# Kernel optimization log

Hardware: AMD Instinct MI355X
Metric: run time of the kernel (lower is better)

Reference implementation:

```python
import jax, jax.numpy as jnp
import numpy as np

N = 20000


def _gcn_conv(x, edge_index, W, b):
    # add self loops
    n = x.shape[0]
    loops = jnp.arange(n, dtype=edge_index.dtype)
    row = jnp.concatenate([edge_index[0], loops])
    col = jnp.concatenate([edge_index[1], loops])
    # linear
    x = x @ W + b  # [N, C_out]
    # symmetric degree norm: deg computed over col (targets)
    deg = jax.ops.segment_sum(jnp.ones_like(col, dtype=x.dtype), col, num_segments=n)
    dinv = jnp.where(deg > 0, deg ** -0.5, 0.0)
    norm = dinv[row] * dinv[col]  # [E+N]
    # gather-scale-scatter (aggr='add' into col)
    msgs = norm[:, None] * x[row]  # [E+N, C_out]
    return jax.ops.segment_sum(msgs, col, num_segments=n)


def setup_inputs() -> dict:
    key = jax.random.key(0)
    k1, k2, k3, k4, k5, k6 = jax.random.split(key, 6)
    in_c, out_c = 256, 128
    hid = 2 * out_c
    x = jax.random.normal(k1, (N, in_c), dtype=jnp.float32)
    edge_index = jax.random.randint(k2, (2, 640000), 0, N, dtype=jnp.int64)
    s1 = 1.0 / np.sqrt(in_c)
    s2 = 1.0 / np.sqrt(hid)
    W1 = jax.random.uniform(k3, (in_c, hid), jnp.float32, -s1, s1)
    b1 = jax.random.uniform(k4, (hid,), jnp.float32, -s1, s1)
    W2 = jax.random.uniform(k5, (hid, out_c), jnp.float32, -s2, s2)
    b2 = jax.random.uniform(k6, (out_c,), jnp.float32, -s2, s2)
    return {"x": x, "edge_index": edge_index, "W1": W1, "b1": b1, "W2": W2, "b2": b2}


def reference(x, edge_index, W1, b1, W2, b2):
    h = jax.nn.relu(_gcn_conv(x, edge_index, W1, b1))
    return _gcn_conv(h, edge_index, W2, b2)
```

## Files before the change

kernel.cpp:

```cpp
#include <hip/hip_runtime.h>

#define CDIV(a,b) (((a)+(b)-1)/(b))

typedef _Float16 half4v __attribute__((ext_vector_type(4)));
typedef _Float16 half2v __attribute__((ext_vector_type(2)));
typedef _Float16 f16x8  __attribute__((ext_vector_type(8)));
typedef unsigned short ushort8v __attribute__((ext_vector_type(8)));
typedef float f32x4 __attribute__((ext_vector_type(4)));

__global__ void prep_kernel(const float* __restrict__ x, _Float16* __restrict__ xh,
                            const float* __restrict__ W1, _Float16* __restrict__ w1t,
                            const float* __restrict__ W2, _Float16* __restrict__ w2t,
                            int* __restrict__ counts,
                            int n, int inc, int hid, int outc) {
    int idx = blockIdx.x * blockDim.x + threadIdx.x;
    int n_xh = n * inc / 8;
    int n_w1 = inc * hid;
    int n_w2 = hid * outc;
    if (idx < n_xh) {
        const float4* xp = (const float4*)(x + (size_t)idx * 8);
        float4 a = xp[0], b = xp[1];
        half4v h0, h1;
        h0.x=(_Float16)a.x; h0.y=(_Float16)a.y; h0.z=(_Float16)a.z; h0.w=(_Float16)a.w;
        h1.x=(_Float16)b.x; h1.y=(_Float16)b.y; h1.z=(_Float16)b.z; h1.w=(_Float16)b.w;
        _Float16* dst = xh + (size_t)idx * 8;
        *(half4v*)dst = h0; *(half4v*)(dst + 4) = h1;
    } else if ((idx -= n_xh) < n_w1) {
        int nr = idx / inc, k = idx - nr * inc;
        w1t[idx] = (_Float16)W1[(size_t)k * hid + nr];
    } else if ((idx -= n_w1) < n_w2) {
        int nr = idx / hid, k = idx - nr * hid;
        w2t[idx] = (_Float16)W2[(size_t)k * outc + nr];
    } else if ((idx -= n_w2) < n) {
        counts[idx] = 0;
    }
}

__global__ void hist_kernel(const int* __restrict__ coli, int* __restrict__ counts, int E) {
    int e = blockIdx.x * blockDim.x + threadIdx.x;
    if (e < E) atomicAdd(&counts[coli[e]], 1);
}

__global__ __launch_bounds__(1024) void scan_part(const int* __restrict__ counts,
                                                  int* __restrict__ offsets,
                                                  int* __restrict__ bsum,
                                                  float* __restrict__ dinv, int n) {
    __shared__ int wsum[16];
    int b = blockIdx.x, tid = threadIdx.x;
    int i = b * 1024 + tid;
    int lane = tid & 63, wid = tid >> 6;
    int v = (i < n) ? counts[i] : 0;
    if (i < n) dinv[i] = 1.0f / sqrtf((float)(v + 1));
    int x = v;
    #pragma unroll
    for (int off = 1; off < 64; off <<= 1) {
        int t = __shfl_up(x, off);
        if (lane >= off) x += t;
    }
    if (lane == 63) wsum[wid] = x;
    __syncthreads();
    if (tid == 0) {
        int run = 0;
        #pragma unroll
        for (int w = 0; w < 16; ++w) { int t = wsum[w]; wsum[w] = run; run += t; }
        bsum[b] = run;
    }
    __syncthreads();
    int incl = wsum[wid] + x;
    if (i < n) offsets[i + 1] = incl;
}

__global__ __launch_bounds__(1024) void scan_fix(const int* __restrict__ counts,
                                                 int* __restrict__ offsets,
                                                 const int* __restrict__ bsum,
                                                 int* __restrict__ nexta, int n) {
    int b = blockIdx.x, tid = threadIdx.x;
    int i = b * 1024 + tid;
    int pre = 0;
    for (int j = 0; j < b; ++j) pre += bsum[j];
    if (i == 0) offsets[0] = 0;
    if (i < n) {
        int incl = offsets[i + 1] + pre;
        offsets[i + 1] = incl;
        nexta[i] = incl - counts[i];
    }
}

__global__ void scatter_kernel(const int* __restrict__ rowi, const int* __restrict__ coli,
                               int* __restrict__ nexta, int* __restrict__ srcs, int E) {
    int e = blockIdx.x * blockDim.x + threadIdx.x;
    if (e < E) {
        int c = coli[e];
        int pos = atomicAdd(&nexta[c], 1);
        srcs[pos] = rowi[e];
    }
}

__global__ void agg1_f16(const _Float16* __restrict__ xh, const int* __restrict__ srcs,
                         const int* __restrict__ offsets, const float* __restrict__ dinv,
                         _Float16* __restrict__ xout, float* __restrict__ sarr,
                         int vpr, int n) {
    int gw   = blockIdx.x * (blockDim.x >> 6) + (threadIdx.x >> 6);
    int lane = threadIdx.x & 63;
    if (gw >= n) return;
    int c   = __builtin_amdgcn_readfirstlane(gw);
    int beg = __builtin_amdgcn_readfirstlane(offsets[c]);
    int end = __builtin_amdgcn_readfirstlane(offsets[c + 1]);
    const half4v* x4 = (const half4v*)xh;
    float4 acc = make_float4(0.f, 0.f, 0.f, 0.f);
    float wsum = 0.f;
    int i = beg;
    for (; i + 3 < end; i += 4) {
        int r0 = __builtin_amdgcn_readfirstlane(srcs[i + 0]);
        int r1 = __builtin_amdgcn_readfirstlane(srcs[i + 1]);
        int r2 = __builtin_amdgcn_readfirstlane(srcs[i + 2]);
        int r3 = __builtin_amdgcn_readfirstlane(srcs[i + 3]);
        float w0 = dinv[r0], w1 = dinv[r1], w2 = dinv[r2], w3 = dinv[r3];
        half4v v0 = x4[(size_t)r0 * vpr + lane];
        half4v v1 = x4[(size_t)r1 * vpr + lane];
        half4v v2 = x4[(size_t)r2 * vpr + lane];
        half4v v3 = x4[(size_t)r3 * vpr + lane];
        acc.x = fmaf(w0, (float)v0.x, acc.x); acc.y = fmaf(w0, (float)v0.y, acc.y);
        acc.z = fmaf(w0, (float)v0.z, acc.z); acc.w = fmaf(w0, (float)v0.w, acc.w);
        acc.x = fmaf(w1, (float)v1.x, acc.x); acc.y = fmaf(w1, (float)v1.y, acc.y);
        acc.z = fmaf(w1, (float)v1.z, acc.z); acc.w = fmaf(w1, (float)v1.w, acc.w);
        acc.x = fmaf(w2, (float)v2.x, acc.x); acc.y = fmaf(w2, (float)v2.y, acc.y);
        acc.z = fmaf(w2, (float)v2.z, acc.z); acc.w = fmaf(w2, (float)v2.w, acc.w);
        acc.x = fmaf(w3, (float)v3.x, acc.x); acc.y = fmaf(w3, (float)v3.y, acc.y);
        acc.z = fmaf(w3, (float)v3.z, acc.z); acc.w = fmaf(w3, (float)v3.w, acc.w);
        wsum += w0 + w1 + w2 + w3;
    }
    for (; i < end; ++i) {
        int r   = __builtin_amdgcn_readfirstlane(srcs[i]);
        float w = dinv[r];
        half4v v = x4[(size_t)r * vpr + lane];
        acc.x = fmaf(w, (float)v.x, acc.x); acc.y = fmaf(w, (float)v.y, acc.y);
        acc.z = fmaf(w, (float)v.z, acc.z); acc.w = fmaf(w, (float)v.w, acc.w);
        wsum += w;
    }
    float dc = dinv[c];
    half4v vc = x4[(size_t)c * vpr + lane];
    acc.x = fmaf(dc, (float)vc.x, acc.x); acc.y = fmaf(dc, (float)vc.y, acc.y);
    acc.z = fmaf(dc, (float)vc.z, acc.z); acc.w = fmaf(dc, (float)vc.w, acc.w);
    wsum += dc;
    half4v o;
    o.x = (_Float16)(acc.x * dc); o.y = (_Float16)(acc.y * dc);
    o.z = (_Float16)(acc.z * dc); o.w = (_Float16)(acc.w * dc);
    ((half4v*)xout)[(size_t)c * vpr + lane] = o;
    if (sarr && lane == 0) sarr[c] = dc * wsum;
}

__global__ void agg2_f16(const _Float16* __restrict__ zh, const int* __restrict__ srcs,
                         const int* __restrict__ offsets, const float* __restrict__ dinv,
                         float* __restrict__ xout, int vpr, int n) {
    int gw   = blockIdx.x * (blockDim.x >> 6) + (threadIdx.x >> 6);
    int lane = threadIdx.x & 63;
    if (gw >= n) return;
    int c   = __builtin_amdgcn_readfirstlane(gw);
    int beg = __builtin_amdgcn_readfirstlane(offsets[c]);
    int end = __builtin_amdgcn_readfirstlane(offsets[c + 1]);
    const half2v* x2 = (const half2v*)zh;
    float2 acc = make_float2(0.f, 0.f);
    int i = beg;
    for (; i + 3 < end; i += 4) {
        int r0 = __builtin_amdgcn_readfirstlane(srcs[i + 0]);
        int r1 = __builtin_amdgcn_readfirstlane(srcs[i + 1]);
        int r2 = __builtin_amdgcn_readfirstlane(srcs[i + 2]);
        int r3 = __builtin_amdgcn_readfirstlane(srcs[i + 3]);
        float w0 = dinv[r0], w1 = dinv[r1], w2 = dinv[r2], w3 = dinv[r3];
        half2v v0 = x2[(size_t)r0 * vpr + lane];
        half2v v1 = x2[(size_t)r1 * vpr + lane];
        half2v v2 = x2[(size_t)r2 * vpr + lane];
        half2v v3 = x2[(size_t)r3 * vpr + lane];
        acc.x = fmaf(w0, (float)v0.x, acc.x); acc.y = fmaf(w0, (float)v0.y, acc.y);
        acc.x = fmaf(w1, (float)v1.x, acc.x); acc.y = fmaf(w1, (float)v1.y, acc.y);
        acc.x = fmaf(w2, (float)v2.x, acc.x); acc.y = fmaf(w2, (float)v2.y, acc.y);
        acc.x = fmaf(w3, (float)v3.x, acc.x); acc.y = fmaf(w3, (float)v3.y, acc.y);
    }
    for (; i < end; ++i) {
        int r   = __builtin_amdgcn_readfirstlane(srcs[i]);
        float w = dinv[r];
        half2v v = x2[(size_t)r * vpr + lane];
        acc.x = fmaf(w, (float)v.x, acc.x); acc.y = fmaf(w, (float)v.y, acc.y);
    }
    float dc = dinv[c];
    half2v vc = x2[(size_t)c * vpr + lane];
    acc.x = fmaf(dc, (float)vc.x, acc.x); acc.y = fmaf(dc, (float)vc.y, acc.y);
    acc.x *= dc; acc.y *= dc;
    ((float2*)xout)[(size_t)c * vpr + lane] = acc;
}

template<int BM, int BN, bool RELU, bool SBIAS>
__global__ __launch_bounds__(256) void gemm_mfma(
        const _Float16* __restrict__ A, const _Float16* __restrict__ BT,
        const float* __restrict__ bias, const float* __restrict__ sarr,
        _Float16* __restrict__ C, int M, int K, int N) {
    constexpr int FM = BM / 2 / 16, FN = BN / 2 / 16;
    constexpr int APT = BM * 4 / 256, BPT = BN * 4 / 256;
    static_assert(BM % 32 == 0 && BN % 32 == 0, "wave tile divisibility");
    __shared__ unsigned short A_lds[BM * 40];
    __shared__ unsigned short B_lds[BN * 40];
    int tid  = threadIdx.x;
    int wid  = tid >> 6, lane = tid & 63;
    int wm   = wid >> 1, wn = wid & 1;
    int q    = lane >> 4, r = lane & 15;
    int m0   = blockIdx.x * BM, n0 = blockIdx.y * BN;

    f32x4 acc[FM][FN];
    #pragma unroll
    for (int i = 0; i < FM; ++i)
        #pragma unroll
        for (int j = 0; j < FN; ++j)
            acc[i][j] = (f32x4){0.f, 0.f, 0.f, 0.f};

    ushort8v areg[APT], breg[BPT];
    auto loadA = [&](int k0) {
        #pragma unroll
        for (int i = 0; i < APT; ++i) {
            int g = tid + i * 256;
            int row = g >> 2, slot = g & 3;
            int gm = m0 + row;
            if (gm < M) areg[i] = *(const ushort8v*)(A + (size_t)gm * K + k0 + slot * 8);
            else        areg[i] = (ushort8v){0,0,0,0,0,0,0,0};
        }
    };
    auto loadB = [&](int k0) {
        #pragma unroll
        for (int i = 0; i < BPT; ++i) {
            int g = tid + i * 256;
            int row = g >> 2, slot = g & 3;
            breg[i] = *(const ushort8v*)(BT + (size_t)(n0 + row) * K + k0 + slot * 8);
        }
    };

    loadA(0); loadB(0);
    int steps = K / 32;
    for (int s = 0; s < steps; ++s) {
        __syncthreads();
        #pragma unroll
        for (int i = 0; i < APT; ++i) {
            int g = tid + i * 256;
            *(ushort8v*)&A_lds[(g >> 2) * 40 + (g & 3) * 8] = areg[i];
        }
        #pragma unroll
        for (int i = 0; i < BPT; ++i) {
            int g = tid + i * 256;
            *(ushort8v*)&B_lds[(g >> 2) * 40 + (g & 3) * 8] = breg[i];
        }
        __syncthreads();
        if (s + 1 < steps) { loadA((s + 1) * 32); loadB((s + 1) * 32); }
        f16x8 af[FM], bf[FN];
        #pragma unroll
        for (int i = 0; i < FM; ++i)
            af[i] = *(const f16x8*)&A_lds[(wm * (BM / 2) + i * 16 + r) * 40 + q * 8];
        #pragma unroll
        for (int j = 0; j < FN; ++j)
            bf[j] = *(const f16x8*)&B_lds[(wn * (BN / 2) + j * 16 + r) * 40 + q * 8];
        #pragma unroll
        for (int i = 0; i < FM; ++i)
            #pragma unroll
            for (int j = 0; j < FN; ++j)
                acc[i][j] = __builtin_amdgcn_mfma_f32_16x16x32_f16(af[i], bf[j], acc[i][j], 0, 0, 0);
    }

    #pragma unroll
    for (int i = 0; i < FM; ++i) {
        int row_base = m0 + wm * (BM / 2) + i * 16 + q * 4;
        #pragma unroll
        for (int g = 0; g < 4; ++g) {
            int row = row_base + g;
            if (row >= M) continue;
            float sv = SBIAS ? sarr[row] : 1.f;
            #pragma unroll
            for (int j = 0; j < FN; ++j) {
                int col = n0 + wn * (BN / 2) + j * 16 + r;
                float v = acc[i][j][g] + sv * bias[col];
                if (RELU) v = fmaxf(v, 0.f);
                C[(size_t)row * N + col] = (_Float16)v;
            }
        }
    }
}

extern "C" void kernel_launch(void* const* d_in, const int* in_sizes, int n_in,
                              void* d_out, int out_size, void* d_ws, size_t ws_size,
                              hipStream_t stream) {
    const float* x  = (const float*)d_in[0];
    const int*   ei = (const int*)d_in[1];
    const float* W1 = (const float*)d_in[2];
    const float* b1 = (const float*)d_in[3];
    const float* W2 = (const float*)d_in[4];
    const float* b2 = (const float*)d_in[5];

    const int hid  = in_sizes[3];
    const int outc = in_sizes[5];
    const int inc  = in_sizes[2] / hid;
    const int n    = in_sizes[0] / inc;
    const int E    = in_sizes[1] / 2;
    const int* rowi = ei;
    const int* coli = ei + E;

    char* p = (char*)d_ws;
    auto carve = [&](size_t bytes) {
        char* q = p;
        p += (bytes + 255) & ~(size_t)255;
        return (void*)q;
    };
    int*      counts  = (int*)     carve((size_t)n * 4);
    int*      offsets = (int*)     carve((size_t)(n + 1) * 4);
    int*      nexta   = (int*)     carve((size_t)n * 4);
    int*      srcs    = (int*)     carve((size_t)(E + 8) * 4);
    float*    dinv    = (float*)   carve((size_t)n * 4);
    float*    sarr    = (float*)   carve((size_t)n * 4);
    int*      bsum    = (int*)     carve((size_t)32 * 4);
    _Float16* xh      = (_Float16*)carve((size_t)n * inc * 2);
    _Float16* aggxh   = (_Float16*)carve((size_t)n * inc * 2);
    _Float16* hh      = (_Float16*)carve((size_t)n * hid * 2);
    _Float16* w1t     = (_Float16*)carve((size_t)inc * hid * 2);
    _Float16* w2t     = (_Float16*)carve((size_t)hid * outc * 2);
    _Float16* zh      = xh;

    const int SCAN_B = CDIV(n, 1024);
    const int PREP_T = n * inc / 8 + inc * hid + hid * outc + n;

    prep_kernel<<<CDIV(PREP_T, 256), 256, 0, stream>>>(x, xh, W1, w1t, W2, w2t, counts,
                                                       n, inc, hid, outc);
    hist_kernel<<<CDIV(E, 256), 256, 0, stream>>>(coli, counts, E);
    scan_part<<<SCAN_B, 1024, 0, stream>>>(counts, offsets, bsum, dinv, n);
    scan_fix<<<SCAN_B, 1024, 0, stream>>>(counts, offsets, bsum, nexta, n);
    scatter_kernel<<<CDIV(E, 256), 256, 0, stream>>>(rowi, coli, nexta, srcs, E);

    agg1_f16<<<CDIV(n, 4), 256, 0, stream>>>(xh, srcs, offsets, dinv, aggxh, sarr, inc / 4, n);
    dim3 g1(CDIV(n, 128), hid / 128);
    gemm_mfma<128, 128, true, true><<<g1, 256, 0, stream>>>(aggxh, w1t, b1, sarr, hh, n, inc, hid);

    dim3 g2(CDIV(n, 64), outc / 128);
    gemm_mfma<64, 128, false, false><<<g2, 256, 0, stream>>>(hh, w2t, b2, nullptr, zh, n, hid, outc);
    agg2_f16<<<CDIV(n, 4), 256, 0, stream>>>(zh, srcs, offsets, dinv, (float*)d_out, outc / 2, n);
}
```

Before: 237.1 us.

## Pack source weight into CSR records and split agg1 columns across two blocks

```diff
diff --git a/kernel.cpp b/kernel.cpp
--- a/kernel.cpp
+++ b/kernel.cpp
@@ -7,6 +7,8 @@
 typedef _Float16 f16x8  __attribute__((ext_vector_type(8)));
 typedef unsigned short ushort8v __attribute__((ext_vector_type(8)));
 typedef float f32x4 __attribute__((ext_vector_type(4)));
+
+#define RL(x) __builtin_amdgcn_readfirstlane(x)
 
 __global__ void prep_kernel(const float* __restrict__ x, _Float16* __restrict__ xh,
                             const float* __restrict__ W1, _Float16* __restrict__ w1t,
@@ -87,87 +89,83 @@
 }
 
 __global__ void scatter_kernel(const int* __restrict__ rowi, const int* __restrict__ coli,
-                               int* __restrict__ nexta, int* __restrict__ srcs, int E) {
+                               const float* __restrict__ dinv,
+                               int* __restrict__ nexta, int2* __restrict__ recs, int E) {
     int e = blockIdx.x * blockDim.x + threadIdx.x;
     if (e < E) {
         int c = coli[e];
+        int r = rowi[e];
         int pos = atomicAdd(&nexta[c], 1);
-        srcs[pos] = rowi[e];
-    }
-}
-
-__global__ void agg1_f16(const _Float16* __restrict__ xh, const int* __restrict__ srcs,
+        recs[pos] = make_int2(r, __float_as_int(dinv[r]));
+    }
+}
+
+__global__ void agg1_f16(const _Float16* __restrict__ xh, const int2* __restrict__ recs,
                          const int* __restrict__ offsets, const float* __restrict__ dinv,
                          _Float16* __restrict__ xout, float* __restrict__ sarr,
-                         int vpr, int n) {
-    int gw   = blockIdx.x * (blockDim.x >> 6) + (threadIdx.x >> 6);
-    int lane = threadIdx.x & 63;
+                         int inc, int n) {
+    int slice = blockIdx.x & 1;
+    int gw    = (blockIdx.x >> 1) * 4 + (threadIdx.x >> 6);
+    int lane  = threadIdx.x & 63;
     if (gw >= n) return;
-    int c   = __builtin_amdgcn_readfirstlane(gw);
-    int beg = __builtin_amdgcn_readfirstlane(offsets[c]);
-    int end = __builtin_amdgcn_readfirstlane(offsets[c + 1]);
-    const half4v* x4 = (const half4v*)xh;
-    float4 acc = make_float4(0.f, 0.f, 0.f, 0.f);
+    int c   = RL(gw);
+    int beg = RL(offsets[c]);
+    int end = RL(offsets[c + 1]);
+    int coff = slice * (inc >> 1) + lane * 2;
+    const _Float16* tab = xh + coff;
+    float2 acc = make_float2(0.f, 0.f);
     float wsum = 0.f;
     int i = beg;
     for (; i + 3 < end; i += 4) {
-        int r0 = __builtin_amdgcn_readfirstlane(srcs[i + 0]);
-        int r1 = __builtin_amdgcn_readfirstlane(srcs[i + 1]);
-        int r2 = __builtin_amdgcn_readfirstlane(srcs[i + 2]);
-        int r3 = __builtin_amdgcn_readfirstlane(srcs[i + 3]);
-        float w0 = dinv[r0], w1 = dinv[r1], w2 = dinv[r2], w3 = dinv[r3];
-        half4v v0 = x4[(size_t)r0 * vpr + lane];
-        half4v v1 = x4[(size_t)r1 * vpr + lane];
-        half4v v2 = x4[(size_t)r2 * vpr + lane];
-        half4v v3 = x4[(size_t)r3 * vpr + lane];
+        int2 a0 = recs[i + 0], a1 = recs[i + 1], a2 = recs[i + 2], a3 = recs[i + 3];
+        int   r0 = RL(a0.x), r1 = RL(a1.x), r2 = RL(a2.x), r3 = RL(a3.x);
+        float w0 = __int_as_float(RL(a0.y)), w1 = __int_as_float(RL(a1.y));
+        float w2 = __int_as_float(RL(a2.y)), w3 = __int_as_float(RL(a3.y));
+        half2v v0 = *(const half2v*)(tab + (size_t)r0 * inc);
+        half2v v1 = *(const half2v*)(tab + (size_t)r1 * inc);
+        half2v v2 = *(const half2v*)(tab + (size_t)r2 * inc);
+        half2v v3 = *(const half2v*)(tab + (size_t)r3 * inc);
         acc.x = fmaf(w0, (float)v0.x, acc.x); acc.y = fmaf(w0, (float)v0.y, acc.y);
-        acc.z = fmaf(w0, (float)v0.z, acc.z); acc.w = fmaf(w0, (float)v0.w, acc.w);
         acc.x = fmaf(w1, (float)v1.x, acc.x); acc.y = fmaf(w1, (float)v1.y, acc.y);
-        acc.z = fmaf(w1, (float)v1.z, acc.z); acc.w = fmaf(w1, (float)v1.w, acc.w);
         acc.x = fmaf(w2, (float)v2.x, acc.x); acc.y = fmaf(w2, (float)v2.y, acc.y);
-        acc.z = fmaf(w2, (float)v2.z, acc.z); acc.w = fmaf(w2, (float)v2.w, acc.w);
         acc.x = fmaf(w3, (float)v3.x, acc.x); acc.y = fmaf(w3, (float)v3.y, acc.y);
-        acc.z = fmaf(w3, (float)v3.z, acc.z); acc.w = fmaf(w3, (float)v3.w, acc.w);
         wsum += w0 + w1 + w2 + w3;
     }
     for (; i < end; ++i) {
-        int r   = __builtin_amdgcn_readfirstlane(srcs[i]);
-        float w = dinv[r];
-        half4v v = x4[(size_t)r * vpr + lane];
+        int2 a = recs[i];
+        int r = RL(a.x);
+        float w = __int_as_float(RL(a.y));
+        half2v v = *(const half2v*)(tab + (size_t)r * inc);
         acc.x = fmaf(w, (float)v.x, acc.x); acc.y = fmaf(w, (float)v.y, acc.y);
-        acc.z = fmaf(w, (float)v.z, acc.z); acc.w = fmaf(w, (float)v.w, acc.w);
         wsum += w;
     }
     float dc = dinv[c];
-    half4v vc = x4[(size_t)c * vpr + lane];
+    half2v vc = *(const half2v*)(tab + (size_t)c * inc);
     acc.x = fmaf(dc, (float)vc.x, acc.x); acc.y = fmaf(dc, (float)vc.y, acc.y);
-    acc.z = fmaf(dc, (float)vc.z, acc.z); acc.w = fmaf(dc, (float)vc.w, acc.w);
     wsum += dc;
-    half4v o;
+    half2v o;
     o.x = (_Float16)(acc.x * dc); o.y = (_Float16)(acc.y * dc);
-    o.z = (_Float16)(acc.z * dc); o.w = (_Float16)(acc.w * dc);
-    ((half4v*)xout)[(size_t)c * vpr + lane] = o;
-    if (sarr && lane == 0) sarr[c] = dc * wsum;
-}
-
-__global__ void agg2_f16(const _Float16* __restrict__ zh, const int* __restrict__ srcs,
+    *(half2v*)(xout + (size_t)c * inc + coff) = o;
+    if (sarr && slice == 0 && lane == 0) sarr[c] = dc * wsum;
+}
+
+__global__ void agg2_f16(const _Float16* __restrict__ zh, const int2* __restrict__ recs,
                          const int* __restrict__ offsets, const float* __restrict__ dinv,
                          float* __restrict__ xout, int vpr, int n) {
     int gw   = blockIdx.x * (blockDim.x >> 6) + (threadIdx.x >> 6);
     int lane = threadIdx.x & 63;
     if (gw >= n) return;
-    int c   = __builtin_amdgcn_readfirstlane(gw);
-    int beg = __builtin_amdgcn_readfirstlane(offsets[c]);
-    int end = __builtin_amdgcn_readfirstlane(offsets[c + 1]);
+    int c   = RL(gw);
+    int beg = RL(offsets[c]);
+    int end = RL(offsets[c + 1]);
     const half2v* x2 = (const half2v*)zh;
     float2 acc = make_float2(0.f, 0.f);
     int i = beg;
     for (; i + 3 < end; i += 4) {
-        int r0 = __builtin_amdgcn_readfirstlane(srcs[i + 0]);
-        int r1 = __builtin_amdgcn_readfirstlane(srcs[i + 1]);
-        int r2 = __builtin_amdgcn_readfirstlane(srcs[i + 2]);
-        int r3 = __builtin_amdgcn_readfirstlane(srcs[i + 3]);
-        float w0 = dinv[r0], w1 = dinv[r1], w2 = dinv[r2], w3 = dinv[r3];
+        int2 a0 = recs[i + 0], a1 = recs[i + 1], a2 = recs[i + 2], a3 = recs[i + 3];
+        int   r0 = RL(a0.x), r1 = RL(a1.x), r2 = RL(a2.x), r3 = RL(a3.x);
+        float w0 = __int_as_float(RL(a0.y)), w1 = __int_as_float(RL(a1.y));
+        float w2 = __int_as_float(RL(a2.y)), w3 = __int_as_float(RL(a3.y));
         half2v v0 = x2[(size_t)r0 * vpr + lane];
         half2v v1 = x2[(size_t)r1 * vpr + lane];
         half2v v2 = x2[(size_t)r2 * vpr + lane];
@@ -178,8 +176,9 @@
         acc.x = fmaf(w3, (float)v3.x, acc.x); acc.y = fmaf(w3, (float)v3.y, acc.y);
     }
     for (; i < end; ++i) {
-        int r   = __builtin_amdgcn_readfirstlane(srcs[i]);
-        float w = dinv[r];
+        int2 a = recs[i];
+        int r = RL(a.x);
+        float w = __int_as_float(RL(a.y));
         half2v v = x2[(size_t)r * vpr + lane];
         acc.x = fmaf(w, (float)v.x, acc.x); acc.y = fmaf(w, (float)v.y, acc.y);
     }
@@ -309,7 +308,7 @@
     int*      counts  = (int*)     carve((size_t)n * 4);
     int*      offsets = (int*)     carve((size_t)(n + 1) * 4);
     int*      nexta   = (int*)     carve((size_t)n * 4);
-    int*      srcs    = (int*)     carve((size_t)(E + 8) * 4);
+    int2*     recs    = (int2*)    carve((size_t)(E + 8) * 8);
     float*    dinv    = (float*)   carve((size_t)n * 4);
     float*    sarr    = (float*)   carve((size_t)n * 4);
     int*      bsum    = (int*)     carve((size_t)32 * 4);
@@ -328,13 +327,13 @@
     hist_kernel<<<CDIV(E, 256), 256, 0, stream>>>(coli, counts, E);
     scan_part<<<SCAN_B, 1024, 0, stream>>>(counts, offsets, bsum, dinv, n);
     scan_fix<<<SCAN_B, 1024, 0, stream>>>(counts, offsets, bsum, nexta, n);
-    scatter_kernel<<<CDIV(E, 256), 256, 0, stream>>>(rowi, coli, nexta, srcs, E);
-
-    agg1_f16<<<CDIV(n, 4), 256, 0, stream>>>(xh, srcs, offsets, dinv, aggxh, sarr, inc / 4, n);
+    scatter_kernel<<<CDIV(E, 256), 256, 0, stream>>>(rowi, coli, dinv, nexta, recs, E);
+
+    agg1_f16<<<CDIV(n, 4) * 2, 256, 0, stream>>>(xh, recs, offsets, dinv, aggxh, sarr, inc, n);
     dim3 g1(CDIV(n, 128), hid / 128);
     gemm_mfma<128, 128, true, true><<<g1, 256, 0, stream>>>(aggxh, w1t, b1, sarr, hh, n, inc, hid);
 
     dim3 g2(CDIV(n, 64), outc / 128);
     gemm_mfma<64, 128, false, false><<<g2, 256, 0, stream>>>(hh, w2t, b2, nullptr, zh, n, hid, outc);
-    agg2_f16<<<CDIV(n, 4), 256, 0, stream>>>(zh, srcs, offsets, dinv, (float*)d_out, outc / 2, n);
-}
+    agg2_f16<<<CDIV(n, 4), 256, 0, stream>>>(zh, recs, offsets, dinv, (float*)d_out, outc / 2, n);
+}
```

Result: no change. 232.9 us (-1.8%).
